# Kernel optimization log

Measured on AMD Instinct MI355X. Metric: run time of the kernel, lower is better.

## Reference

```python
import jax, jax.numpy as jnp
from jax import lax
import numpy as np

S, B, I, H = 1024, 512, 5, 32
G = 4 * H  # torch LSTM gate dim, order: i, f, g, o


def setup_inputs() -> dict:
    key = jax.random.key(0)
    ks = jax.random.split(key, 19)
    n = lambda k, shape, s=0.1: jax.random.normal(k, shape, jnp.float32) * s
    return {
        "x": jax.random.normal(ks[0], (S, B, I), jnp.float32),
        "Wih0": n(ks[1], (G, I)), "Whh0": n(ks[2], (G, H)), "bih0": n(ks[3], (G,)), "bhh0": n(ks[4], (G,)),
        "Wih1": n(ks[5], (G, H)), "Whh1": n(ks[6], (G, H)), "bih1": n(ks[7], (G,)), "bhh1": n(ks[8], (G,)),
        "Wih2": n(ks[9], (G, H)), "Whh2": n(ks[10], (G, H)), "bih2": n(ks[11], (G,)), "bhh2": n(ks[12], (G,)),
        "w1": n(ks[13], (H, H)), "b1": n(ks[14], (H,)),
        "w2": n(ks[15], (H, H)), "b2": n(ks[16], (H,)),
        "w3": n(ks[17], (1, H)), "b3": n(ks[18], (1,)),
    }


def lstm_layer(x, Wih, Whh, bih, bhh):
    # x: [S, B, in]; precompute input projections for all steps (one big GEMM)
    xp = jnp.einsum("sbi,gi->sbg", x, Wih) + bih + bhh  # [S, B, 4H]
    h0 = jnp.zeros((x.shape[1], H), x.dtype)
    c0 = jnp.zeros((x.shape[1], H), x.dtype)

    def step(carry, xg):
        h, c = carry
        gates = xg + h @ Whh.T  # [B, 4H]
        i, f, g, o = jnp.split(gates, 4, axis=-1)
        c = jax.nn.sigmoid(f) * c + jax.nn.sigmoid(i) * jnp.tanh(g)
        h = jax.nn.sigmoid(o) * jnp.tanh(c)
        return (h, c), h

    _, ys = lax.scan(step, (h0, c0), xp)
    return ys  # [S, B, H]


def reference(x, Wih0, Whh0, bih0, bhh0, Wih1, Whh1, bih1, bhh1,
              Wih2, Whh2, bih2, bhh2, w1, b1, w2, b2, w3, b3):
    h = lstm_layer(x, Wih0, Whh0, bih0, bhh0)
    h = lstm_layer(h, Wih1, Whh1, bih1, bhh1)
    h = lstm_layer(h, Wih2, Whh2, bih2, bhh2)  # [S, B, H]
    s, b, hd = h.shape
    y = h.reshape(s * b, hd)
    y = y @ w1.T + b1
    y = y @ w2.T + b2
    y = y @ w3.T + b3
    y = jax.nn.relu(y)
    return y.reshape(s, b, -1)  # [S, B, 1]
```

## Files before the change

kernel.cpp:

```cpp
#include <hip/hip_runtime.h>
#include <math.h>

#define S_LEN  1024
#define BATCH  512
#define HID    32
#define RING_D 8

__device__ __forceinline__ float fast_rcp(float x) { return __builtin_amdgcn_rcpf(x); }

__device__ __forceinline__ float sigmoid_f(float x) {
    return fast_rcp(1.0f + __expf(-x));
}

__device__ __forceinline__ float tanh_f(float x) {
    float t = __expf(-2.0f * fabsf(x));
    float r = (1.0f - t) * fast_rcp(1.0f + t);
    return copysignf(r, x);
}

__device__ __forceinline__ float rl(float v, int k) {
    return __int_as_float(__builtin_amdgcn_readlane(__float_as_int(v), k));
}

__global__ __launch_bounds__(192)
void lstm3_async(const float* __restrict__ x,
                 const float* __restrict__ Wih0, const float* __restrict__ Whh0,
                 const float* __restrict__ bih0, const float* __restrict__ bhh0,
                 const float* __restrict__ Wih1, const float* __restrict__ Whh1,
                 const float* __restrict__ bih1, const float* __restrict__ bhh1,
                 const float* __restrict__ Wih2, const float* __restrict__ Whh2,
                 const float* __restrict__ bih2, const float* __restrict__ bhh2,
                 const float* __restrict__ w1, const float* __restrict__ b1,
                 const float* __restrict__ w2, const float* __restrict__ b2,
                 const float* __restrict__ w3, const float* __restrict__ b3,
                 float* __restrict__ out)
{
    const int b = blockIdx.x;
    const int w = threadIdx.x >> 6;
    const int l = threadIdx.x & 63;
    const int j = l & 31;
    const bool lowHalf = (l < 32);
    const int gA = l;
    const int gB = l + 64;

    __shared__ float xlds[S_LEN * 5];
    __shared__ float ring[2][RING_D][HID];
    __shared__ int   flg[2][RING_D];
    __shared__ int   prog[2];

    {
        const float* xb = x + (size_t)b * 5;
        for (int i = threadIdx.x; i < S_LEN * 5; i += 192) {
            int s = i / 5;
            int k = i - 5 * s;
            xlds[i] = xb[(size_t)s * (BATCH * 5) + k];
        }
    }
    if (threadIdx.x < 2 * RING_D) (&flg[0][0])[threadIdx.x] = 0;
    if (threadIdx.x < 2) prog[threadIdx.x] = 0;
    __syncthreads();

    const float* Wih = (w == 0) ? Wih0 : (w == 1) ? Wih1 : Wih2;
    const float* Whh = (w == 0) ? Whh0 : (w == 1) ? Whh1 : Whh2;
    const float* bih = (w == 0) ? bih0 : (w == 1) ? bih1 : bih2;
    const float* bhh = (w == 0) ? bhh0 : (w == 1) ? bhh1 : bhh2;

    float whhA[HID], whhB[HID];
#pragma unroll
    for (int k = 0; k < HID; ++k) {
        whhA[k] = Whh[gA * HID + k];
        whhB[k] = Whh[gB * HID + k];
    }
    float wihA[HID], wihB[HID];
    if (w == 0) {
#pragma unroll
        for (int k = 0; k < 5; ++k) {
            wihA[k] = Wih[gA * 5 + k];
            wihB[k] = Wih[gB * 5 + k];
        }
    } else {
#pragma unroll
        for (int k = 0; k < HID; ++k) {
            wihA[k] = Wih[gA * HID + k];
            wihB[k] = Wih[gB * HID + k];
        }
    }
    const float biasA = bih[gA] + bhh[gA];
    const float biasB = bih[gB] + bhh[gB];

    float u_own = 0.0f, beta = 0.0f;
    if (w == 2) {
        float t_own = 0.0f;
#pragma unroll
        for (int k = 0; k < HID; ++k)
            t_own += w3[k] * w2[k * HID + j];
        float uo = 0.0f, bt = 0.0f;
#pragma unroll
        for (int k = 0; k < HID; ++k) {
            float tk = rl(t_own, k);
            uo += tk * w1[k * HID + j];
            bt += tk * b1[k] + w3[k] * b2[k];
        }
        u_own = uo;
        beta = bt + b3[0];
    }

    float c = 0.0f;
    float h = 0.0f;

    for (int s = 0; s < S_LEN; ++s) {
        const int slot = s & (RING_D - 1);

        float aA0 = biasA, aA1 = 0.f, aA2 = 0.f, aA3 = 0.f;
        float aB0 = biasB, aB1 = 0.f, aB2 = 0.f, aB3 = 0.f;
#pragma unroll
        for (int k = 0; k < HID; k += 4) {
            float h0 = rl(h, k + 0);
            float h1 = rl(h, k + 1);
            float h2 = rl(h, k + 2);
            float h3 = rl(h, k + 3);
            aA0 += whhA[k + 0] * h0;  aB0 += whhB[k + 0] * h0;
            aA1 += whhA[k + 1] * h1;  aB1 += whhB[k + 1] * h1;
            aA2 += whhA[k + 2] * h2;  aB2 += whhB[k + 2] * h2;
            aA3 += whhA[k + 3] * h3;  aB3 += whhB[k + 3] * h3;
        }

        if (w == 0) {
            const float* xs = &xlds[s * 5];
            float x0 = xs[0], x1 = xs[1], x2 = xs[2], x3 = xs[3], x4 = xs[4];
            aA0 += wihA[0] * x0 + wihA[4] * x4;
            aB0 += wihB[0] * x0 + wihB[4] * x4;
            aA1 += wihA[1] * x1;  aB1 += wihB[1] * x1;
            aA2 += wihA[2] * x2;  aB2 += wihB[2] * x2;
            aA3 += wihA[3] * x3;  aB3 += wihB[3] * x3;
        } else {
            while (__hip_atomic_load(&flg[w - 1][slot], __ATOMIC_ACQUIRE,
                                     __HIP_MEMORY_SCOPE_WORKGROUP) != s + 1) {}
            const float4* r4 = reinterpret_cast<const float4*>(&ring[w - 1][slot][0]);
#pragma unroll
            for (int k4 = 0; k4 < HID / 4; ++k4) {
                float4 hv = r4[k4];
                aA0 += wihA[4 * k4 + 0] * hv.x;  aB0 += wihB[4 * k4 + 0] * hv.x;
                aA1 += wihA[4 * k4 + 1] * hv.y;  aB1 += wihB[4 * k4 + 1] * hv.y;
                aA2 += wihA[4 * k4 + 2] * hv.z;  aB2 += wihB[4 * k4 + 2] * hv.z;
                aA3 += wihA[4 * k4 + 3] * hv.w;  aB3 += wihB[4 * k4 + 3] * hv.w;
            }
            if (l == 0)
                __hip_atomic_store(&prog[w - 1], s + 1, __ATOMIC_RELEASE,
                                   __HIP_MEMORY_SCOPE_WORKGROUP);
        }
        float accA = (aA0 + aA1) + (aA2 + aA3);
        float accB = (aB0 + aB1) + (aB2 + aB3);

        float pA = __shfl_xor(accA, 32);
        float pB = __shfl_xor(accB, 32);
        float gi = lowHalf ? accA : pA;
        float gf = lowHalf ? pA : accA;
        float gg = lowHalf ? accB : pB;
        float go = lowHalf ? pB : accB;

        gi = sigmoid_f(gi);
        gf = sigmoid_f(gf);
        gg = tanh_f(gg);
        go = sigmoid_f(go);
        c = gf * c + gi * gg;
        h = go * tanh_f(c);

        if (w < 2) {
            if (s >= RING_D) {
                while (__hip_atomic_load(&prog[w], __ATOMIC_ACQUIRE,
                                         __HIP_MEMORY_SCOPE_WORKGROUP)
                       < s - (RING_D - 1)) {}
            }
            if (lowHalf) ring[w][slot][j] = h;
            if (l == 0)
                __hip_atomic_store(&flg[w][slot], s + 1, __ATOMIC_RELEASE,
                                   __HIP_MEMORY_SCOPE_WORKGROUP);
        } else {
            float prt = u_own * h;
            prt += __shfl_xor(prt, 1);
            prt += __shfl_xor(prt, 2);
            prt += __shfl_xor(prt, 4);
            prt += __shfl_xor(prt, 8);
            prt += __shfl_xor(prt, 16);
            if (l == 0) out[(size_t)s * BATCH + b] = fmaxf(prt + beta, 0.0f);
        }
    }
}

extern "C" void kernel_launch(void* const* d_in, const int* in_sizes, int n_in,
                              void* d_out, int out_size, void* d_ws, size_t ws_size,
                              hipStream_t stream)
{
    const float* x    = (const float*)d_in[0];
    const float* Wih0 = (const float*)d_in[1];
    const float* Whh0 = (const float*)d_in[2];
    const float* bih0 = (const float*)d_in[3];
    const float* bhh0 = (const float*)d_in[4];
    const float* Wih1 = (const float*)d_in[5];
    const float* Whh1 = (const float*)d_in[6];
    const float* bih1 = (const float*)d_in[7];
    const float* bhh1 = (const float*)d_in[8];
    const float* Wih2 = (const float*)d_in[9];
    const float* Whh2 = (const float*)d_in[10];
    const float* bih2 = (const float*)d_in[11];
    const float* bhh2 = (const float*)d_in[12];
    const float* w1   = (const float*)d_in[13];
    const float* b1   = (const float*)d_in[14];
    const float* w2   = (const float*)d_in[15];
    const float* b2   = (const float*)d_in[16];
    const float* w3   = (const float*)d_in[17];
    const float* b3   = (const float*)d_in[18];

    lstm3_async<<<BATCH, 192, 0, stream>>>(x, Wih0, Whh0, bih0, bhh0,
                                           Wih1, Whh1, bih1, bhh1,
                                           Wih2, Whh2, bih2, bhh2,
                                           w1, b1, w2, b2, w3, b3,
                                           (float*)d_out);
}
```

Before: 994.4 us.

## Process two batch elements per workgroup to fill idle half-wave lanes

Each workgroup now handles two batch elements. Each wave lane computes gate pre-activations for both sequences, reusing its register-resident weights, and the half-wave shuffle is rearranged so each half of the wave owns one sequence's cell state. This uses the lanes that previously duplicated work and halves the grid to 256 blocks. In exchange, each step's serial dependency chain roughly doubles in FMA count, so per-step latency grows and fewer CUs are occupied.

```diff
diff --git a/kernel.cpp b/kernel.cpp
--- a/kernel.cpp
+++ b/kernel.cpp
@@ -22,38 +22,39 @@
     return __int_as_float(__builtin_amdgcn_readlane(__float_as_int(v), k));
 }
 
-__global__ __launch_bounds__(192)
-void lstm3_async(const float* __restrict__ x,
-                 const float* __restrict__ Wih0, const float* __restrict__ Whh0,
-                 const float* __restrict__ bih0, const float* __restrict__ bhh0,
-                 const float* __restrict__ Wih1, const float* __restrict__ Whh1,
-                 const float* __restrict__ bih1, const float* __restrict__ bhh1,
-                 const float* __restrict__ Wih2, const float* __restrict__ Whh2,
-                 const float* __restrict__ bih2, const float* __restrict__ bhh2,
-                 const float* __restrict__ w1, const float* __restrict__ b1,
-                 const float* __restrict__ w2, const float* __restrict__ b2,
-                 const float* __restrict__ w3, const float* __restrict__ b3,
-                 float* __restrict__ out)
+__global__ __launch_bounds__(192, 1)
+void lstm3_x2(const float* __restrict__ x,
+              const float* __restrict__ Wih0, const float* __restrict__ Whh0,
+              const float* __restrict__ bih0, const float* __restrict__ bhh0,
+              const float* __restrict__ Wih1, const float* __restrict__ Whh1,
+              const float* __restrict__ bih1, const float* __restrict__ bhh1,
+              const float* __restrict__ Wih2, const float* __restrict__ Whh2,
+              const float* __restrict__ bih2, const float* __restrict__ bhh2,
+              const float* __restrict__ w1, const float* __restrict__ b1,
+              const float* __restrict__ w2, const float* __restrict__ b2,
+              const float* __restrict__ w3, const float* __restrict__ b3,
+              float* __restrict__ out)
 {
-    const int b = blockIdx.x;
+    const int blk = blockIdx.x;
     const int w = threadIdx.x >> 6;
     const int l = threadIdx.x & 63;
     const int j = l & 31;
-    const bool lowHalf = (l < 32);
+    const int half = l >> 5;
+    const bool lowHalf = (half == 0);
     const int gA = l;
     const int gB = l + 64;
 
-    __shared__ float xlds[S_LEN * 5];
-    __shared__ float ring[2][RING_D][HID];
+    __shared__ float xlds[S_LEN * 10];
+    __shared__ float ring[2][RING_D][2][HID];
     __shared__ int   flg[2][RING_D];
     __shared__ int   prog[2];
 
     {
-        const float* xb = x + (size_t)b * 5;
-        for (int i = threadIdx.x; i < S_LEN * 5; i += 192) {
-            int s = i / 5;
-            int k = i - 5 * s;
-            xlds[i] = xb[(size_t)s * (BATCH * 5) + k];
+        const float* xb = x + (size_t)blk * 10;
+        for (int i = threadIdx.x; i < S_LEN * 10; i += 192) {
+            int s = i / 10;
+            int r = i - 10 * s;
+            xlds[i] = xb[(size_t)s * (BATCH * 5) + r];
         }
     }
     if (threadIdx.x < 2 * RING_D) (&flg[0][0])[threadIdx.x] = 0;
@@ -111,53 +112,70 @@
     for (int s = 0; s < S_LEN; ++s) {
         const int slot = s & (RING_D - 1);
 
-        float aA0 = biasA, aA1 = 0.f, aA2 = 0.f, aA3 = 0.f;
-        float aB0 = biasB, aB1 = 0.f, aB2 = 0.f, aB3 = 0.f;
-#pragma unroll
-        for (int k = 0; k < HID; k += 4) {
-            float h0 = rl(h, k + 0);
-            float h1 = rl(h, k + 1);
-            float h2 = rl(h, k + 2);
-            float h3 = rl(h, k + 3);
-            aA0 += whhA[k + 0] * h0;  aB0 += whhB[k + 0] * h0;
-            aA1 += whhA[k + 1] * h1;  aB1 += whhB[k + 1] * h1;
-            aA2 += whhA[k + 2] * h2;  aB2 += whhB[k + 2] * h2;
-            aA3 += whhA[k + 3] * h3;  aB3 += whhB[k + 3] * h3;
-        }
-
-        if (w == 0) {
-            const float* xs = &xlds[s * 5];
-            float x0 = xs[0], x1 = xs[1], x2 = xs[2], x3 = xs[3], x4 = xs[4];
-            aA0 += wihA[0] * x0 + wihA[4] * x4;
-            aB0 += wihB[0] * x0 + wihB[4] * x4;
-            aA1 += wihA[1] * x1;  aB1 += wihB[1] * x1;
-            aA2 += wihA[2] * x2;  aB2 += wihB[2] * x2;
-            aA3 += wihA[3] * x3;  aB3 += wihB[3] * x3;
-        } else {
+        float4 hinA[HID / 4], hinB[HID / 4];
+        if (w > 0) {
             while (__hip_atomic_load(&flg[w - 1][slot], __ATOMIC_ACQUIRE,
                                      __HIP_MEMORY_SCOPE_WORKGROUP) != s + 1) {}
-            const float4* r4 = reinterpret_cast<const float4*>(&ring[w - 1][slot][0]);
+            const float4* rA = reinterpret_cast<const float4*>(&ring[w - 1][slot][0][0]);
+            const float4* rB = reinterpret_cast<const float4*>(&ring[w - 1][slot][1][0]);
+#pragma unroll
+            for (int k4 = 0; k4 < HID / 4; ++k4) { hinA[k4] = rA[k4]; hinB[k4] = rB[k4]; }
+        }
+
+        float aA0_A = biasA, aA1_A = 0.f, aB0_A = biasB, aB1_A = 0.f;
+        float aA0_B = biasA, aA1_B = 0.f, aB0_B = biasB, aB1_B = 0.f;
+#pragma unroll
+        for (int k = 0; k < HID; k += 2) {
+            float hA0 = rl(h, k);      float hA1 = rl(h, k + 1);
+            float hB0 = rl(h, k + 32); float hB1 = rl(h, k + 33);
+            aA0_A += whhA[k] * hA0;  aA1_A += whhA[k + 1] * hA1;
+            aB0_A += whhB[k] * hA0;  aB1_A += whhB[k + 1] * hA1;
+            aA0_B += whhA[k] * hB0;  aA1_B += whhA[k + 1] * hB1;
+            aB0_B += whhB[k] * hB0;  aB1_B += whhB[k + 1] * hB1;
+        }
+
+        if (w == 0) {
+            const float* xs = &xlds[s * 10];
+            float xA0 = xs[0], xA1 = xs[1], xA2 = xs[2], xA3 = xs[3], xA4 = xs[4];
+            float xB0 = xs[5], xB1 = xs[6], xB2 = xs[7], xB3 = xs[8], xB4 = xs[9];
+            aA0_A += wihA[0] * xA0 + wihA[2] * xA2 + wihA[4] * xA4;
+            aA1_A += wihA[1] * xA1 + wihA[3] * xA3;
+            aB0_A += wihB[0] * xA0 + wihB[2] * xA2 + wihB[4] * xA4;
+            aB1_A += wihB[1] * xA1 + wihB[3] * xA3;
+            aA0_B += wihA[0] * xB0 + wihA[2] * xB2 + wihA[4] * xB4;
+            aA1_B += wihA[1] * xB1 + wihA[3] * xB3;
+            aB0_B += wihB[0] * xB0 + wihB[2] * xB2 + wihB[4] * xB4;
+            aB1_B += wihB[1] * xB1 + wihB[3] * xB3;
+        } else {
 #pragma unroll
             for (int k4 = 0; k4 < HID / 4; ++k4) {
-                float4 hv = r4[k4];
-                aA0 += wihA[4 * k4 + 0] * hv.x;  aB0 += wihB[4 * k4 + 0] * hv.x;
-                aA1 += wihA[4 * k4 + 1] * hv.y;  aB1 += wihB[4 * k4 + 1] * hv.y;
-                aA2 += wihA[4 * k4 + 2] * hv.z;  aB2 += wihB[4 * k4 + 2] * hv.z;
-                aA3 += wihA[4 * k4 + 3] * hv.w;  aB3 += wihB[4 * k4 + 3] * hv.w;
+                float4 hA = hinA[k4], hB = hinB[k4];
+                aA0_A += wihA[4*k4+0] * hA.x;  aA1_A += wihA[4*k4+1] * hA.y;
+                aA0_A += wihA[4*k4+2] * hA.z;  aA1_A += wihA[4*k4+3] * hA.w;
+                aB0_A += wihB[4*k4+0] * hA.x;  aB1_A += wihB[4*k4+1] * hA.y;
+                aB0_A += wihB[4*k4+2] * hA.z;  aB1_A += wihB[4*k4+3] * hA.w;
+                aA0_B += wihA[4*k4+0] * hB.x;  aA1_B += wihA[4*k4+1] * hB.y;
+                aA0_B += wihA[4*k4+2] * hB.z;  aA1_B += wihA[4*k4+3] * hB.w;
+                aB0_B += wihB[4*k4+0] * hB.x;  aB1_B += wihB[4*k4+1] * hB.y;
+                aB0_B += wihB[4*k4+2] * hB.z;  aB1_B += wihB[4*k4+3] * hB.w;
             }
             if (l == 0)
                 __hip_atomic_store(&prog[w - 1], s + 1, __ATOMIC_RELEASE,
                                    __HIP_MEMORY_SCOPE_WORKGROUP);
         }
-        float accA = (aA0 + aA1) + (aA2 + aA3);
-        float accB = (aB0 + aB1) + (aB2 + aB3);
-
-        float pA = __shfl_xor(accA, 32);
-        float pB = __shfl_xor(accB, 32);
-        float gi = lowHalf ? accA : pA;
-        float gf = lowHalf ? pA : accA;
-        float gg = lowHalf ? accB : pB;
-        float go = lowHalf ? pB : accB;
+        float accA_A = aA0_A + aA1_A;
+        float accB_A = aB0_A + aB1_A;
+        float accA_B = aA0_B + aA1_B;
+        float accB_B = aB0_B + aB1_B;
+
+        float v1 = lowHalf ? accA_B : accA_A;
+        float r1 = __shfl_xor(v1, 32);
+        float v2 = lowHalf ? accB_B : accB_A;
+        float r2 = __shfl_xor(v2, 32);
+        float gi = lowHalf ? accA_A : r1;
+        float gf = lowHalf ? r1 : accA_B;
+        float gg = lowHalf ? accB_A : r2;
+        float go = lowHalf ? r2 : accB_B;
 
         gi = sigmoid_f(gi);
         gf = sigmoid_f(gf);
@@ -172,7 +190,7 @@
                                          __HIP_MEMORY_SCOPE_WORKGROUP)
                        < s - (RING_D - 1)) {}
             }
-            if (lowHalf) ring[w][slot][j] = h;
+            ring[w][slot][half][j] = h;
             if (l == 0)
                 __hip_atomic_store(&flg[w][slot], s + 1, __ATOMIC_RELEASE,
                                    __HIP_MEMORY_SCOPE_WORKGROUP);
@@ -183,7 +201,8 @@
             prt += __shfl_xor(prt, 4);
             prt += __shfl_xor(prt, 8);
             prt += __shfl_xor(prt, 16);
-            if (l == 0) out[(size_t)s * BATCH + b] = fmaxf(prt + beta, 0.0f);
+            if ((l & 31) == 0)
+                out[(size_t)s * BATCH + 2 * blk + half] = fmaxf(prt + beta, 0.0f);
         }
     }
 }
@@ -212,9 +231,9 @@
     const float* w3   = (const float*)d_in[17];
     const float* b3   = (const float*)d_in[18];
 
-    lstm3_async<<<BATCH, 192, 0, stream>>>(x, Wih0, Whh0, bih0, bhh0,
-                                           Wih1, Whh1, bih1, bhh1,
-                                           Wih2, Whh2, bih2, bhh2,
-                                           w1, b1, w2, b2, w3, b3,
-                                           (float*)d_out);
-}
+    lstm3_x2<<<BATCH / 2, 192, 0, stream>>>(x, Wih0, Whh0, bih0, bhh0,
+                                            Wih1, Whh1, bih1, bhh1,
+                                            Wih2, Whh2, bih2, bhh2,
+                                            w1, b1, w2, b2, w3, b3,
+                                            (float*)d_out);
+}
```

Result: slower. 1.075 ms (+8.1%).
